# Optimization experiments

Measured on AMD Instinct MI355X. Metric: run time of the kernel, lower is better.

The kernel has to match this reference:

```python
import jax, jax.numpy as jnp
import numpy as np

V, D, H, L, FF, C = 32000, 512, 8, 3, 2048, 6
B, S = 32, 1024


def setup_inputs() -> dict:
    key = jax.random.key(0)
    ks = jax.random.split(key, 8)
    tokens = jax.random.randint(ks[0], (B, S), 0, V, dtype=jnp.int32)
    emb = jax.random.normal(ks[1], (V, D), dtype=jnp.float32) * 0.02
    qkv_w = jax.random.normal(ks[2], (L, D, 3 * D), dtype=jnp.float32) * (D ** -0.5)
    qkv_b = jnp.zeros((L, 3 * D), dtype=jnp.float32)
    fc_w = jax.random.normal(ks[3], (L, D, D), dtype=jnp.float32) * (D ** -0.5)
    fc_b = jnp.zeros((L, D), dtype=jnp.float32)
    gamma = jnp.ones((D,), dtype=jnp.float32)
    beta = jnp.zeros((D,), dtype=jnp.float32)
    fc1_w = jax.random.normal(ks[4], (D, FF), dtype=jnp.float32) * (D ** -0.5)
    fc1_b = jnp.zeros((FF,), dtype=jnp.float32)
    fc2_w = jax.random.normal(ks[5], (FF, C), dtype=jnp.float32) * (FF ** -0.5)
    fc2_b = jnp.zeros((C,), dtype=jnp.float32)
    return dict(tokens=tokens, emb=emb, qkv_w=qkv_w, qkv_b=qkv_b, fc_w=fc_w,
                fc_b=fc_b, gamma=gamma, beta=beta, fc1_w=fc1_w, fc1_b=fc1_b,
                fc2_w=fc2_w, fc2_b=fc2_b)


def _sinusoidal_pe(seq_len, dim):
    pos = jnp.arange(seq_len, dtype=jnp.float32)[:, None]
    div = jnp.exp(jnp.arange(0, dim, 2).astype(jnp.float32) * (-np.log(10000.0) / dim))
    pe = jnp.zeros((seq_len, dim), dtype=jnp.float32)
    pe = pe.at[:, 0::2].set(jnp.sin(pos * div))
    pe = pe.at[:, 1::2].set(jnp.cos(pos * div))
    return pe


def reference(tokens, emb, qkv_w, qkv_b, fc_w, fc_b, gamma, beta, fc1_w, fc1_b, fc2_w, fc2_b):
    b, s = tokens.shape
    dh = D // H
    scale = dh ** -0.5

    def layernorm(y):
        m = y.mean(-1, keepdims=True)
        v = ((y - m) ** 2).mean(-1, keepdims=True)
        return (y - m) * jax.lax.rsqrt(v + 1e-5) * gamma + beta

    x = emb[tokens] + _sinusoidal_pe(s, D)[None]  # [B,S,D]
    for l in range(L):
        qkv = (x @ qkv_w[l] + qkv_b[l]).reshape(b, s, H, 3, dh)
        q = qkv[..., 0, :].transpose(0, 2, 1, 3)  # [B,H,S,dh]
        k = qkv[..., 1, :].transpose(0, 2, 1, 3)
        v = qkv[..., 2, :].transpose(0, 2, 1, 3)
        attn = jax.nn.softmax(jnp.einsum('bhqd,bhkd->bhqk', q, k) * scale, axis=-1)
        o = jnp.einsum('bhqk,bhkd->bhqd', attn, v).transpose(0, 2, 1, 3).reshape(b, s, D)
        o = o @ fc_w[l] + fc_b[l]
        x = layernorm(o + x)
    pooled = x.mean(axis=1)  # [B,D]
    h = jax.nn.relu(pooled @ fc1_w + fc1_b)  # dropout is identity at inference
    return h @ fc2_w + fc2_b
```

## Files before the change

### kernel.cpp

```cpp
#include <hip/hip_runtime.h>
#include <cmath>

#define BS_TOK 32768
#define DMODEL 512
#define NHEAD 8
#define DHEAD 64
#define NLAYER 3
#define FFDIM 2048
#define NCLS 6
#define BATCH 32
#define SEQ 1024
#define QKVW 1536

typedef short short8 __attribute__((ext_vector_type(8)));
typedef float float4v __attribute__((ext_vector_type(4)));
typedef unsigned int uint4v __attribute__((ext_vector_type(4)));
#define MFMA_BF16 __builtin_amdgcn_mfma_f32_16x16x32_bf16
#define QSCALE 0.18033688011112042f

__device__ __forceinline__ unsigned short f2bf(float x) {
    return (unsigned short)((__float_as_uint(x) + 0x8000u) >> 16);
}

__device__ __forceinline__ unsigned int cvt_pk_bf16(float a, float b) {
    unsigned int r;
    asm("v_cvt_pk_bf16_f32 %0, %1, %2" : "=v"(r) : "v"(a), "v"(b));
    return r;
}

#define PL32(a, b) asm("v_permlane32_swap_b32 %0, %1" : "+v"(a), "+v"(b))
#define PL16(a, b) asm("v_permlane16_swap_b32 %0, %1" : "+v"(a), "+v"(b))

__global__ __launch_bounds__(128) void embed_pe_kernel(const int* __restrict__ tokens,
                                                       const float* __restrict__ emb,
                                                       float* __restrict__ X,
                                                       unsigned short* __restrict__ Xb) {
    int t = blockIdx.x;
    int pos = t & (SEQ - 1);
    int tok = tokens[t];
    int d0 = threadIdx.x * 4;
    float4 e = *(const float4*)(emb + (size_t)tok * DMODEL + d0);
    const float c = -9.210340371976184f / 512.0f;
    float div0 = expf((float)d0 * c);
    float div1 = expf((float)(d0 + 2) * c);
    float a0 = (float)pos * div0;
    float a1 = (float)pos * div1;
    e.x += sinf(a0); e.y += cosf(a0);
    e.z += sinf(a1); e.w += cosf(a1);
    *(float4*)(X + (size_t)t * DMODEL + d0) = e;
    *(ushort4*)(Xb + (size_t)t * DMODEL + d0) =
        make_ushort4(f2bf(e.x), f2bf(e.y), f2bf(e.z), f2bf(e.w));
}

__global__ __launch_bounds__(256) void transcvt_kernel(const float* __restrict__ in,
                                                       unsigned short* __restrict__ out,
                                                       int R, int C) {
    __shared__ float t[32][33];
    size_t base = (size_t)blockIdx.z * R * C;
    int c0 = blockIdx.x * 32, r0 = blockIdx.y * 32;
    int tx = threadIdx.x & 31, ty = threadIdx.x >> 5;
#pragma unroll
    for (int i = 0; i < 4; i++)
        t[ty + i * 8][tx] = in[base + (size_t)(r0 + ty + i * 8) * C + c0 + tx];
    __syncthreads();
#pragma unroll
    for (int i = 0; i < 4; i++)
        out[base + (size_t)(c0 + ty + i * 8) * R + r0 + tx] = f2bf(t[tx][ty + i * 8]);
}

__global__ __launch_bounds__(256) void transcvt_qkv_kernel(const float* __restrict__ in,
                                                           unsigned short* __restrict__ out) {
    __shared__ float t[32][33];
    int l = blockIdx.z;
    int n0 = blockIdx.x * 32, r0 = blockIdx.y * 32;
    int seg = n0 >> 9, nn = n0 & 511, h = nn >> 6, d0 = nn & 63;
    int c0 = h * 192 + seg * 64 + d0;
    float s = (seg == 0) ? QSCALE : 1.f;
    const float* inp = in + (size_t)l * DMODEL * QKVW;
    unsigned short* op = out + (size_t)l * QKVW * DMODEL;
    int tx = threadIdx.x & 31, ty = threadIdx.x >> 5;
#pragma unroll
    for (int i = 0; i < 4; i++)
        t[ty + i * 8][tx] = inp[(size_t)(r0 + ty + i * 8) * QKVW + c0 + tx];
    __syncthreads();
#pragma unroll
    for (int i = 0; i < 4; i++)
        op[(size_t)(n0 + ty + i * 8) * DMODEL + r0 + tx] = f2bf(t[tx][ty + i * 8] * s);
}

__global__ __launch_bounds__(256) void permbias_kernel(const float* __restrict__ qkv_b,
                                                       float* __restrict__ pb) {
    int i = blockIdx.x * 256 + threadIdx.x;
    int l = i / QKVW, n = i - l * QKVW;
    int seg = n >> 9, nn = n & 511, h = nn >> 6, d = nn & 63;
    float s = (seg == 0) ? QSCALE : 1.f;
    pb[i] = qkv_b[l * QKVW + h * 192 + seg * 64 + d] * s;
}

__global__ __launch_bounds__(256, 3) void gemm_qkv_kernel(const unsigned short* __restrict__ A,
                                                          const unsigned short* __restrict__ Bt,
                                                          const float* __restrict__ pb,
                                                          unsigned short* __restrict__ QKc,
                                                          unsigned short* __restrict__ Vt,
                                                          int M) {
    __shared__ unsigned short As[128 * 40];
    __shared__ unsigned short Bs[128 * 40];
    int bm = blockIdx.y * 128, bn = blockIdx.x * 128;
    int tid = threadIdx.x;
    int w = tid >> 6, lane = tid & 63, l15 = lane & 15, quad = lane >> 4;
    int wm = (w & 1) * 64, wn = (w >> 1) * 64;

    float4v acc[4][4];
    float4v z = {0.f, 0.f, 0.f, 0.f};
#pragma unroll
    for (int i = 0; i < 4; i++)
#pragma unroll
        for (int j = 0; j < 4; j++) acc[i][j] = z;

    int r0 = tid >> 2, o0 = (tid & 3) * 8;
    int r1 = (tid + 256) >> 2, o1 = (tid & 3) * 8;

    for (int k0 = 0; k0 < DMODEL; k0 += 32) {
        __syncthreads();
        *(short8*)&As[r0 * 40 + o0] = *(const short8*)(A + (size_t)(bm + r0) * DMODEL + k0 + o0);
        *(short8*)&As[r1 * 40 + o1] = *(const short8*)(A + (size_t)(bm + r1) * DMODEL + k0 + o1);
        *(short8*)&Bs[r0 * 40 + o0] = *(const short8*)(Bt + (size_t)(bn + r0) * DMODEL + k0 + o0);
        *(short8*)&Bs[r1 * 40 + o1] = *(const short8*)(Bt + (size_t)(bn + r1) * DMODEL + k0 + o1);
        __syncthreads();
        short8 af[4], bf[4];
#pragma unroll
        for (int i = 0; i < 4; i++)
            af[i] = *(short8*)&As[(wm + i * 16 + l15) * 40 + quad * 8];
#pragma unroll
        for (int j = 0; j < 4; j++)
            bf[j] = *(short8*)&Bs[(wn + j * 16 + l15) * 40 + quad * 8];
#pragma unroll
        for (int i = 0; i < 4; i++)
#pragma unroll
            for (int j = 0; j < 4; j++)
                acc[i][j] = MFMA_BF16(af[i], bf[j], acc[i][j], 0, 0, 0);
    }

    float bj[4];
#pragma unroll
    for (int j = 0; j < 4; j++) bj[j] = pb[bn + wn + j * 16 + l15];

    if (bn < 1024) {
#pragma unroll
        for (int i = 0; i < 4; i++)
#pragma unroll
            for (int r = 0; r < 4; r++) {
                size_t row = (size_t)(bm + wm + i * 16 + quad * 4 + r);
#pragma unroll
                for (int j = 0; j < 4; j++)
                    QKc[row * 1024 + bn + wn + j * 16 + l15] = f2bf(acc[i][j][r] + bj[j]);
            }
    } else {
        int bl = bm >> 10;
        int sbase = (bm & 1023) + wm;
#pragma unroll
        for (int j = 0; j < 4; j++) {
            int colp = bn - 1024 + wn + j * 16 + l15;
            int h = colp >> 6, d = colp & 63;
            unsigned short* vb = Vt + ((size_t)(bl * 8 + h) * 64 + d) * 1024 + sbase;
#pragma unroll
            for (int i = 0; i < 4; i++) {
                ushort4 v4 = make_ushort4(f2bf(acc[i][j][0] + bj[j]),
                                          f2bf(acc[i][j][1] + bj[j]),
                                          f2bf(acc[i][j][2] + bj[j]),
                                          f2bf(acc[i][j][3] + bj[j]));
                *(ushort4*)(vb + i * 16 + quad * 4) = v4;
            }
        }
    }
}

__global__ __launch_bounds__(256, 2) void attn_kernel(const unsigned short* __restrict__ QKc,
                                                      const unsigned short* __restrict__ Vt,
                                                      unsigned short* __restrict__ O) {
    __shared__ unsigned short Ks[64 * 72];
    __shared__ unsigned short Vts[64 * 72];
    int bh = blockIdx.y;
    int b = bh >> 3, h = bh & 7;
    int q0 = blockIdx.x * 256;
    int tid = threadIdx.x;
    int w = tid >> 6, lane = tid & 63, l15 = lane & 15, quad = lane >> 4;
    const unsigned short* Kg = QKc + (size_t)b * SEQ * 1024 + 512 + h * 64;
    const unsigned short* Vg = Vt + (size_t)bh * 64 * 1024;

    short8 qf[4][2];
#pragma unroll
    for (int i = 0; i < 4; i++) {
        const unsigned short* qb =
            QKc + (size_t)(b * SEQ + q0 + w * 64 + i * 16 + l15) * 1024 + h * 64;
        qf[i][0] = *(const short8*)(qb + quad * 8);
        qf[i][1] = *(const short8*)(qb + 32 + quad * 8);
    }

    float lsum[4] = {0.f, 0.f, 0.f, 0.f};
    float4v accO[4][4];
    float4v z = {0.f, 0.f, 0.f, 0.f};
#pragma unroll
    for (int i = 0; i < 4; i++)
#pragma unroll
        for (int dc = 0; dc < 4; dc++) accO[i][dc] = z;

    int sr = tid >> 2, so = (tid & 3) * 16;

    short8 kp0, kp1, vp0, vp1;
    {
        const unsigned short* kg = Kg + (size_t)sr * 1024 + so;
        kp0 = *(const short8*)kg;
        kp1 = *(const short8*)(kg + 8);
        const unsigned short* vg = Vg + (size_t)sr * 1024 + so;
        vp0 = *(const short8*)vg;
        vp1 = *(const short8*)(vg + 8);
    }

    for (int jt = 0; jt < SEQ / 64; jt++) {
        __syncthreads();
        *(short8*)&Ks[sr * 72 + so] = kp0;
        *(short8*)&Ks[sr * 72 + so + 8] = kp1;
        *(short8*)&Vts[sr * 72 + so] = vp0;
        *(short8*)&Vts[sr * 72 + so + 8] = vp1;
        __syncthreads();

        if (jt + 1 < SEQ / 64) {
            const unsigned short* kg = Kg + (size_t)((jt + 1) * 64 + sr) * 1024 + so;
            kp0 = *(const short8*)kg;
            kp1 = *(const short8*)(kg + 8);
            const unsigned short* vg = Vg + (size_t)sr * 1024 + (jt + 1) * 64 + so;
            vp0 = *(const short8*)vg;
            vp1 = *(const short8*)(vg + 8);
        }

        short8 pa[4][2];
#pragma unroll
        for (int f = 0; f < 2; f++) {
            float4v st[4][2];
#pragma unroll
            for (int jj = 0; jj < 2; jj++) {
                int jc = f * 2 + jj;
                short8 kf0 = *(short8*)&Ks[(jc * 16 + l15) * 72 + quad * 8];
                short8 kf1 = *(short8*)&Ks[(jc * 16 + l15) * 72 + 32 + quad * 8];
#pragma unroll
                for (int i = 0; i < 4; i++) {
                    float4v s0 = MFMA_BF16(kf0, qf[i][0], z, 0, 0, 0);
                    st[i][jj] = MFMA_BF16(kf1, qf[i][1], s0, 0, 0, 0);
                }
            }
#pragma unroll
            for (int i = 0; i < 4; i++) {
                unsigned int pk[4];
#pragma unroll
                for (int jj = 0; jj < 2; jj++) {
                    float p0 = exp2f(st[i][jj][0]);
                    float p1 = exp2f(st[i][jj][1]);
                    float p2 = exp2f(st[i][jj][2]);
                    float p3 = exp2f(st[i][jj][3]);
                    lsum[i] += (p0 + p1) + (p2 + p3);
                    pk[jj * 2 + 0] = cvt_pk_bf16(p0, p1);
                    pk[jj * 2 + 1] = cvt_pk_bf16(p2, p3);
                }
                PL32(pk[0], pk[2]);
                PL32(pk[1], pk[3]);
                PL16(pk[0], pk[2]);
                PL16(pk[1], pk[3]);
                uint4v t;
                t[0] = pk[0]; t[1] = pk[1]; t[2] = pk[2]; t[3] = pk[3];
                pa[i][f] = __builtin_bit_cast(short8, t);
            }
        }

        __builtin_amdgcn_s_setprio(1);
#pragma unroll
        for (int dc = 0; dc < 4; dc++) {
            short8 vf0 = *(short8*)&Vts[(dc * 16 + l15) * 72 + quad * 8];
            short8 vf1 = *(short8*)&Vts[(dc * 16 + l15) * 72 + 32 + quad * 8];
#pragma unroll
            for (int i = 0; i < 4; i++) {
                accO[i][dc] = MFMA_BF16(pa[i][0], vf0, accO[i][dc], 0, 0, 0);
                accO[i][dc] = MFMA_BF16(pa[i][1], vf1, accO[i][dc], 0, 0, 0);
            }
        }
        __builtin_amdgcn_s_setprio(0);
    }

#pragma unroll
    for (int i = 0; i < 4; i++) {
        float s = lsum[i];
        s += __shfl_xor(s, 16);
        s += __shfl_xor(s, 32);
#pragma unroll
        for (int r = 0; r < 4; r++) {
            float rinv = 1.f / __shfl(s, quad * 4 + r);
            size_t row = (size_t)(b * SEQ + q0 + w * 64 + i * 16 + quad * 4 + r);
#pragma unroll
            for (int dc = 0; dc < 4; dc++)
                O[row * DMODEL + h * DHEAD + dc * 16 + l15] = f2bf(accO[i][dc][r] * rinv);
        }
    }
}

__global__ __launch_bounds__(256, 2) void proj_ln_kernel(const unsigned short* __restrict__ A,
                                                         const unsigned short* __restrict__ Bt,
                                                         const float* __restrict__ bias,
                                                         const float* __restrict__ gamma,
                                                         const float* __restrict__ beta,
                                                         float* __restrict__ X,
                                                         unsigned short* __restrict__ Xb) {
    __shared__ unsigned short As[32 * 40];
    __shared__ unsigned short Bs[512 * 40];
    __shared__ float redS[4][32], redQ[4][32];
    int bm = blockIdx.x * 32;
    int tid = threadIdx.x;
    int w = tid >> 6, lane = tid & 63, l15 = lane & 15, quad = lane >> 4;
    int wn = w * 128;

    float4v acc[2][8];
    float4v z = {0.f, 0.f, 0.f, 0.f};
#pragma unroll
    for (int i = 0; i < 2; i++)
#pragma unroll
        for (int j = 0; j < 8; j++) acc[i][j] = z;

    for (int k0 = 0; k0 < DMODEL; k0 += 32) {
        __syncthreads();
        if (tid < 128) {
            int r = tid >> 2, o = (tid & 3) * 8;
            *(short8*)&As[r * 40 + o] = *(const short8*)(A + (size_t)(bm + r) * DMODEL + k0 + o);
        }
#pragma unroll
        for (int u = 0; u < 8; u++) {
            int c = tid + u * 256;
            int r = c >> 2, o = (c & 3) * 8;
            *(short8*)&Bs[r * 40 + o] = *(const short8*)(Bt + (size_t)r * DMODEL + k0 + o);
        }
        __syncthreads();
        short8 af[2];
#pragma unroll
        for (int i = 0; i < 2; i++)
            af[i] = *(short8*)&As[(i * 16 + l15) * 40 + quad * 8];
#pragma unroll
        for (int j = 0; j < 8; j++) {
            short8 bf = *(short8*)&Bs[(wn + j * 16 + l15) * 40 + quad * 8];
            acc[0][j] = MFMA_BF16(af[0], bf, acc[0][j], 0, 0, 0);
            acc[1][j] = MFMA_BF16(af[1], bf, acc[1][j], 0, 0, 0);
        }
    }

    float bj[8], g[8], be[8];
#pragma unroll
    for (int j = 0; j < 8; j++) {
        int col = wn + j * 16 + l15;
        bj[j] = bias[col]; g[j] = gamma[col]; be[j] = beta[col];
    }

    float o[2][4][8];
#pragma unroll
    for (int i = 0; i < 2; i++)
#pragma unroll
        for (int r = 0; r < 4; r++) {
            int lrow = i * 16 + quad * 4 + r;
            size_t row = (size_t)(bm + lrow);
            float ss = 0.f, qq = 0.f;
#pragma unroll
            for (int j = 0; j < 8; j++) {
                float v = acc[i][j][r] + bj[j] + X[row * DMODEL + wn + j * 16 + l15];
                o[i][r][j] = v; ss += v; qq += v * v;
            }
#pragma unroll
            for (int mask = 1; mask < 16; mask <<= 1) {
                ss += __shfl_xor(ss, mask);
                qq += __shfl_xor(qq, mask);
            }
            if (l15 == 0) { redS[w][lrow] = ss; redQ[w][lrow] = qq; }
        }
    __syncthreads();
#pragma unroll
    for (int i = 0; i < 2; i++)
#pragma unroll
        for (int r = 0; r < 4; r++) {
            int lrow = i * 16 + quad * 4 + r;
            float S = redS[0][lrow] + redS[1][lrow] + redS[2][lrow] + redS[3][lrow];
            float Q = redQ[0][lrow] + redQ[1][lrow] + redQ[2][lrow] + redQ[3][lrow];
            float mean = S * (1.f / 512.f);
            float var = Q * (1.f / 512.f) - mean * mean;
            float rstd = rsqrtf(var + 1e-5f);
            size_t row = (size_t)(bm + lrow);
#pragma unroll
            for (int j = 0; j < 8; j++) {
                float n = (o[i][r][j] - mean) * rstd * g[j] + be[j];
                X[row * DMODEL + wn + j * 16 + l15] = n;
                Xb[row * DMODEL + wn + j * 16 + l15] = f2bf(n);
            }
        }
}

__global__ __launch_bounds__(256) void zero_kernel(float* __restrict__ p) {
    p[blockIdx.x * 256 + threadIdx.x] = 0.f;
}
__global__ __launch_bounds__(128) void pool_kernel(const float* __restrict__ X,
                                                   float* __restrict__ pooled) {
    int b = blockIdx.x, ch = blockIdx.y;
    int d0 = threadIdx.x * 4;
    float4 acc = make_float4(0.f, 0.f, 0.f, 0.f);
    const float* base = X + (size_t)(b * SEQ + ch * 64) * DMODEL + d0;
    for (int s2 = 0; s2 < 64; s2++) {
        float4 v = *(const float4*)(base + (size_t)s2 * DMODEL);
        acc.x += v.x; acc.y += v.y; acc.z += v.z; acc.w += v.w;
    }
    atomicAdd(pooled + b * DMODEL + d0 + 0, acc.x);
    atomicAdd(pooled + b * DMODEL + d0 + 1, acc.y);
    atomicAdd(pooled + b * DMODEL + d0 + 2, acc.z);
    atomicAdd(pooled + b * DMODEL + d0 + 3, acc.w);
}

__global__ __launch_bounds__(256) void fc1_kernel(const float* __restrict__ pooled,
                                                  const float* __restrict__ fc1_w,
                                                  const float* __restrict__ fc1_b,
                                                  float* __restrict__ h) {
    __shared__ float p[DMODEL];
    int ffc = blockIdx.x, b = blockIdx.y;
    int tid = threadIdx.x;
    p[tid] = pooled[b * DMODEL + tid] * (1.f / 1024.f);
    p[tid + 256] = pooled[b * DMODEL + tid + 256] * (1.f / 1024.f);
    __syncthreads();
    int ff = ffc * 256 + tid;
    float acc = fc1_b[ff];
    for (int k = 0; k < DMODEL; k++) acc += p[k] * fc1_w[(size_t)k * FFDIM + ff];
    h[(size_t)b * FFDIM + ff] = fmaxf(acc, 0.f);
}

__global__ __launch_bounds__(256) void fc2_kernel(const float* __restrict__ h,
                                                  const float* __restrict__ fc2_w,
                                                  const float* __restrict__ fc2_b,
                                                  float* __restrict__ out) {
    __shared__ float red[NCLS][256];
    int b = blockIdx.x, tid = threadIdx.x;
    float a[NCLS];
#pragma unroll
    for (int c = 0; c < NCLS; c++) a[c] = 0.f;
    int k0 = tid * 8;
#pragma unroll
    for (int u = 0; u < 8; u++) {
        float hv = h[(size_t)b * FFDIM + k0 + u];
#pragma unroll
        for (int c = 0; c < NCLS; c++) a[c] += hv * fc2_w[(k0 + u) * NCLS + c];
    }
#pragma unroll
    for (int c = 0; c < NCLS; c++) red[c][tid] = a[c];
    __syncthreads();
    if (tid < NCLS) {
        float s = 0.f;
        for (int i = 0; i < 256; i++) s += red[tid][i];
        out[b * NCLS + tid] = s + fc2_b[tid];
    }
}

extern "C" void kernel_launch(void* const* d_in, const int* in_sizes, int n_in,
                              void* d_out, int out_size, void* d_ws, size_t ws_size,
                              hipStream_t stream) {
    const int* tokens = (const int*)d_in[0];
    const float* emb = (const float*)d_in[1];
    const float* qkv_w = (const float*)d_in[2];
    const float* qkv_b = (const float*)d_in[3];
    const float* fc_w = (const float*)d_in[4];
    const float* fc_b = (const float*)d_in[5];
    const float* gamma = (const float*)d_in[6];
    const float* beta = (const float*)d_in[7];
    const float* fc1_w = (const float*)d_in[8];
    const float* fc1_b = (const float*)d_in[9];
    const float* fc2_w = (const float*)d_in[10];
    const float* fc2_b = (const float*)d_in[11];
    float* out = (float*)d_out;

    char* p = (char*)d_ws;
    float* X = (float*)p;                         p += (size_t)BS_TOK * DMODEL * 4;
    unsigned short* Xb = (unsigned short*)p;      p += (size_t)BS_TOK * DMODEL * 2;
    float* pooled = (float*)p;                    p += (size_t)BATCH * DMODEL * 4;
    float* hbuf = (float*)p;                      p += (size_t)BATCH * FFDIM * 4;
    float* pb = (float*)p;                        p += (size_t)NLAYER * QKVW * 4;
    unsigned short* qkv_wbt = (unsigned short*)p; p += (size_t)NLAYER * QKVW * DMODEL * 2;
    unsigned short* fc_wt = (unsigned short*)p;   p += (size_t)NLAYER * DMODEL * DMODEL * 2;
    size_t fixed_bytes = (size_t)(p - (char*)d_ws);
    size_t per_batch = (size_t)SEQ * 1024 * 2 + (size_t)NHEAD * 64 * SEQ * 2
                     + (size_t)SEQ * DMODEL * 2;
    int chunkB = 1;
    for (int cb = 32; cb >= 1; cb >>= 1)
        if (fixed_bytes + (size_t)cb * per_batch <= ws_size) { chunkB = cb; break; }
    unsigned short* QKc = (unsigned short*)p;     p += (size_t)chunkB * SEQ * 1024 * 2;
    unsigned short* Vt = (unsigned short*)p;      p += (size_t)chunkB * NHEAD * 64 * SEQ * 2;
    unsigned short* Oc = (unsigned short*)p;
    int rows = chunkB * SEQ;
    int nchunks = BATCH / chunkB;

    embed_pe_kernel<<<BS_TOK, 128, 0, stream>>>(tokens, emb, X, Xb);
    permbias_kernel<<<NLAYER * QKVW / 256, 256, 0, stream>>>(qkv_b, pb);
    transcvt_qkv_kernel<<<dim3(QKVW / 32, DMODEL / 32, NLAYER), 256, 0, stream>>>(
        qkv_w, qkv_wbt);
    transcvt_kernel<<<dim3(DMODEL / 32, DMODEL / 32, NLAYER), 256, 0, stream>>>(
        fc_w, fc_wt, DMODEL, DMODEL);

    for (int l = 0; l < NLAYER; l++) {
        for (int c = 0; c < nchunks; c++) {
            unsigned short* Xbc = Xb + (size_t)c * rows * DMODEL;
            float* Xc = X + (size_t)c * rows * DMODEL;
            gemm_qkv_kernel<<<dim3(QKVW / 128, rows / 128), 256, 0, stream>>>(
                Xbc, qkv_wbt + (size_t)l * QKVW * DMODEL, pb + (size_t)l * QKVW,
                QKc, Vt, rows);
            attn_kernel<<<dim3(SEQ / 256, chunkB * NHEAD), 256, 0, stream>>>(QKc, Vt, Oc);
            proj_ln_kernel<<<rows / 32, 256, 0, stream>>>(
                Oc, fc_wt + (size_t)l * DMODEL * DMODEL, fc_b + (size_t)l * DMODEL,
                gamma, beta, Xc, Xbc);
        }
    }

    zero_kernel<<<BATCH * DMODEL / 256, 256, 0, stream>>>(pooled);
    pool_kernel<<<dim3(BATCH, 16), 128, 0, stream>>>(X, pooled);
    fc1_kernel<<<dim3(FFDIM / 256, BATCH), 256, 0, stream>>>(pooled, fc1_w, fc1_b, hbuf);
    fc2_kernel<<<BATCH, 256, 0, stream>>>(hbuf, fc2_w, fc2_b, out);
}
```

Baseline: 941.4 us.

## Double-buffer LDS in QKV GEMM and attention, interleave softmax with PV MFMAs

```diff
diff --git a/kernel.cpp b/kernel.cpp
--- a/kernel.cpp
+++ b/kernel.cpp
@@ -103,8 +103,8 @@
                                                           unsigned short* __restrict__ QKc,
                                                           unsigned short* __restrict__ Vt,
                                                           int M) {
-    __shared__ unsigned short As[128 * 40];
-    __shared__ unsigned short Bs[128 * 40];
+    __shared__ unsigned short As[2][128 * 40];
+    __shared__ unsigned short Bs[2][128 * 40];
     int bm = blockIdx.y * 128, bn = blockIdx.x * 128;
     int tid = threadIdx.x;
     int w = tid >> 6, lane = tid & 63, l15 = lane & 15, quad = lane >> 4;
@@ -118,27 +118,45 @@
         for (int j = 0; j < 4; j++) acc[i][j] = z;
 
     int r0 = tid >> 2, o0 = (tid & 3) * 8;
-    int r1 = (tid + 256) >> 2, o1 = (tid & 3) * 8;
+    int r1 = (tid + 256) >> 2;
+
+    const unsigned short* Ar0 = A + (size_t)(bm + r0) * DMODEL + o0;
+    const unsigned short* Ar1 = A + (size_t)(bm + r1) * DMODEL + o0;
+    const unsigned short* Br0 = Bt + (size_t)(bn + r0) * DMODEL + o0;
+    const unsigned short* Br1 = Bt + (size_t)(bn + r1) * DMODEL + o0;
+
+    short8 a0 = *(const short8*)Ar0;
+    short8 a1 = *(const short8*)Ar1;
+    short8 b0 = *(const short8*)Br0;
+    short8 b1 = *(const short8*)Br1;
 
     for (int k0 = 0; k0 < DMODEL; k0 += 32) {
+        unsigned short* Ac = As[(k0 >> 5) & 1];
+        unsigned short* Bc = Bs[(k0 >> 5) & 1];
+        *(short8*)&Ac[r0 * 40 + o0] = a0;
+        *(short8*)&Ac[r1 * 40 + o0] = a1;
+        *(short8*)&Bc[r0 * 40 + o0] = b0;
+        *(short8*)&Bc[r1 * 40 + o0] = b1;
         __syncthreads();
-        *(short8*)&As[r0 * 40 + o0] = *(const short8*)(A + (size_t)(bm + r0) * DMODEL + k0 + o0);
-        *(short8*)&As[r1 * 40 + o1] = *(const short8*)(A + (size_t)(bm + r1) * DMODEL + k0 + o1);
-        *(short8*)&Bs[r0 * 40 + o0] = *(const short8*)(Bt + (size_t)(bn + r0) * DMODEL + k0 + o0);
-        *(short8*)&Bs[r1 * 40 + o1] = *(const short8*)(Bt + (size_t)(bn + r1) * DMODEL + k0 + o1);
-        __syncthreads();
+        int kn = (k0 + 32 < DMODEL) ? k0 + 32 : k0;
+        a0 = *(const short8*)(Ar0 + kn);
+        a1 = *(const short8*)(Ar1 + kn);
+        b0 = *(const short8*)(Br0 + kn);
+        b1 = *(const short8*)(Br1 + kn);
         short8 af[4], bf[4];
 #pragma unroll
         for (int i = 0; i < 4; i++)
-            af[i] = *(short8*)&As[(wm + i * 16 + l15) * 40 + quad * 8];
+            af[i] = *(short8*)&Ac[(wm + i * 16 + l15) * 40 + quad * 8];
 #pragma unroll
         for (int j = 0; j < 4; j++)
-            bf[j] = *(short8*)&Bs[(wn + j * 16 + l15) * 40 + quad * 8];
+            bf[j] = *(short8*)&Bc[(wn + j * 16 + l15) * 40 + quad * 8];
+        __builtin_amdgcn_s_setprio(1);
 #pragma unroll
         for (int i = 0; i < 4; i++)
 #pragma unroll
             for (int j = 0; j < 4; j++)
                 acc[i][j] = MFMA_BF16(af[i], bf[j], acc[i][j], 0, 0, 0);
+        __builtin_amdgcn_s_setprio(0);
     }
 
     float bj[4];
@@ -178,8 +196,8 @@
 __global__ __launch_bounds__(256, 2) void attn_kernel(const unsigned short* __restrict__ QKc,
                                                       const unsigned short* __restrict__ Vt,
                                                       unsigned short* __restrict__ O) {
-    __shared__ unsigned short Ks[64 * 72];
-    __shared__ unsigned short Vts[64 * 72];
+    __shared__ unsigned short Ks[2][64 * 72];
+    __shared__ unsigned short Vts[2][64 * 72];
     int bh = blockIdx.y;
     int b = bh >> 3, h = bh & 7;
     int q0 = blockIdx.x * 256;
@@ -217,71 +235,115 @@
         vp1 = *(const short8*)(vg + 8);
     }
 
-    for (int jt = 0; jt < SEQ / 64; jt++) {
+    const int NT = SEQ / 64;
+    for (int jt = 0; jt < NT; jt++) {
+        unsigned short* Kc = Ks[jt & 1];
+        unsigned short* Vc = Vts[jt & 1];
+        *(short8*)&Kc[sr * 72 + so] = kp0;
+        *(short8*)&Kc[sr * 72 + so + 8] = kp1;
+        *(short8*)&Vc[sr * 72 + so] = vp0;
+        *(short8*)&Vc[sr * 72 + so + 8] = vp1;
         __syncthreads();
-        *(short8*)&Ks[sr * 72 + so] = kp0;
-        *(short8*)&Ks[sr * 72 + so + 8] = kp1;
-        *(short8*)&Vts[sr * 72 + so] = vp0;
-        *(short8*)&Vts[sr * 72 + so + 8] = vp1;
-        __syncthreads();
-
-        if (jt + 1 < SEQ / 64) {
-            const unsigned short* kg = Kg + (size_t)((jt + 1) * 64 + sr) * 1024 + so;
+
+        {
+            int nj = (jt + 1 < NT) ? jt + 1 : jt;
+            const unsigned short* kg = Kg + (size_t)(nj * 64 + sr) * 1024 + so;
             kp0 = *(const short8*)kg;
             kp1 = *(const short8*)(kg + 8);
-            const unsigned short* vg = Vg + (size_t)sr * 1024 + (jt + 1) * 64 + so;
+            const unsigned short* vg = Vg + (size_t)sr * 1024 + nj * 64 + so;
             vp0 = *(const short8*)vg;
             vp1 = *(const short8*)(vg + 8);
         }
 
-        short8 pa[4][2];
-#pragma unroll
-        for (int f = 0; f < 2; f++) {
-            float4v st[4][2];
+        float4v st0[4][2];
+        __builtin_amdgcn_s_setprio(1);
+#pragma unroll
+        for (int jj = 0; jj < 2; jj++) {
+            short8 kf0 = *(short8*)&Kc[(jj * 16 + l15) * 72 + quad * 8];
+            short8 kf1 = *(short8*)&Kc[(jj * 16 + l15) * 72 + 32 + quad * 8];
+#pragma unroll
+            for (int i = 0; i < 4; i++) {
+                float4v s0 = MFMA_BF16(kf0, qf[i][0], z, 0, 0, 0);
+                st0[i][jj] = MFMA_BF16(kf1, qf[i][1], s0, 0, 0, 0);
+            }
+        }
+        __builtin_amdgcn_s_setprio(0);
+
+        short8 pa0[4];
+#pragma unroll
+        for (int i = 0; i < 4; i++) {
+            unsigned int pk[4];
 #pragma unroll
             for (int jj = 0; jj < 2; jj++) {
-                int jc = f * 2 + jj;
-                short8 kf0 = *(short8*)&Ks[(jc * 16 + l15) * 72 + quad * 8];
-                short8 kf1 = *(short8*)&Ks[(jc * 16 + l15) * 72 + 32 + quad * 8];
-#pragma unroll
-                for (int i = 0; i < 4; i++) {
-                    float4v s0 = MFMA_BF16(kf0, qf[i][0], z, 0, 0, 0);
-                    st[i][jj] = MFMA_BF16(kf1, qf[i][1], s0, 0, 0, 0);
-                }
-            }
+                float p0 = exp2f(st0[i][jj][0]);
+                float p1 = exp2f(st0[i][jj][1]);
+                float p2 = exp2f(st0[i][jj][2]);
+                float p3 = exp2f(st0[i][jj][3]);
+                lsum[i] += (p0 + p1) + (p2 + p3);
+                pk[jj * 2 + 0] = cvt_pk_bf16(p0, p1);
+                pk[jj * 2 + 1] = cvt_pk_bf16(p2, p3);
+            }
+            PL32(pk[0], pk[2]);
+            PL32(pk[1], pk[3]);
+            PL16(pk[0], pk[2]);
+            PL16(pk[1], pk[3]);
+            uint4v t;
+            t[0] = pk[0]; t[1] = pk[1]; t[2] = pk[2]; t[3] = pk[3];
+            pa0[i] = __builtin_bit_cast(short8, t);
+        }
+
+        float4v st1[4][2];
+        __builtin_amdgcn_s_setprio(1);
+#pragma unroll
+        for (int jj = 0; jj < 2; jj++) {
+            short8 kf0 = *(short8*)&Kc[((2 + jj) * 16 + l15) * 72 + quad * 8];
+            short8 kf1 = *(short8*)&Kc[((2 + jj) * 16 + l15) * 72 + 32 + quad * 8];
 #pragma unroll
             for (int i = 0; i < 4; i++) {
-                unsigned int pk[4];
-#pragma unroll
-                for (int jj = 0; jj < 2; jj++) {
-                    float p0 = exp2f(st[i][jj][0]);
-                    float p1 = exp2f(st[i][jj][1]);
-                    float p2 = exp2f(st[i][jj][2]);
-                    float p3 = exp2f(st[i][jj][3]);
-                    lsum[i] += (p0 + p1) + (p2 + p3);
-                    pk[jj * 2 + 0] = cvt_pk_bf16(p0, p1);
-                    pk[jj * 2 + 1] = cvt_pk_bf16(p2, p3);
-                }
-                PL32(pk[0], pk[2]);
-                PL32(pk[1], pk[3]);
-                PL16(pk[0], pk[2]);
-                PL16(pk[1], pk[3]);
-                uint4v t;
-                t[0] = pk[0]; t[1] = pk[1]; t[2] = pk[2]; t[3] = pk[3];
-                pa[i][f] = __builtin_bit_cast(short8, t);
-            }
+                float4v s0 = MFMA_BF16(kf0, qf[i][0], z, 0, 0, 0);
+                st1[i][jj] = MFMA_BF16(kf1, qf[i][1], s0, 0, 0, 0);
+            }
+        }
+
+#pragma unroll
+        for (int dc = 0; dc < 4; dc++) {
+            short8 vf0 = *(short8*)&Vc[(dc * 16 + l15) * 72 + quad * 8];
+#pragma unroll
+            for (int i = 0; i < 4; i++)
+                accO[i][dc] = MFMA_BF16(pa0[i], vf0, accO[i][dc], 0, 0, 0);
+        }
+        __builtin_amdgcn_s_setprio(0);
+
+        short8 pa1[4];
+#pragma unroll
+        for (int i = 0; i < 4; i++) {
+            unsigned int pk[4];
+#pragma unroll
+            for (int jj = 0; jj < 2; jj++) {
+                float p0 = exp2f(st1[i][jj][0]);
+                float p1 = exp2f(st1[i][jj][1]);
+                float p2 = exp2f(st1[i][jj][2]);
+                float p3 = exp2f(st1[i][jj][3]);
+                lsum[i] += (p0 + p1) + (p2 + p3);
+                pk[jj * 2 + 0] = cvt_pk_bf16(p0, p1);
+                pk[jj * 2 + 1] = cvt_pk_bf16(p2, p3);
+            }
+            PL32(pk[0], pk[2]);
+            PL32(pk[1], pk[3]);
+            PL16(pk[0], pk[2]);
+            PL16(pk[1], pk[3]);
+            uint4v t;
+            t[0] = pk[0]; t[1] = pk[1]; t[2] = pk[2]; t[3] = pk[3];
+            pa1[i] = __builtin_bit_cast(short8, t);
         }
 
         __builtin_amdgcn_s_setprio(1);
 #pragma unroll
         for (int dc = 0; dc < 4; dc++) {
-            short8 vf0 = *(short8*)&Vts[(dc * 16 + l15) * 72 + quad * 8];
-            short8 vf1 = *(short8*)&Vts[(dc * 16 + l15) * 72 + 32 + quad * 8];
-#pragma unroll
-            for (int i = 0; i < 4; i++) {
-                accO[i][dc] = MFMA_BF16(pa[i][0], vf0, accO[i][dc], 0, 0, 0);
-                accO[i][dc] = MFMA_BF16(pa[i][1], vf1, accO[i][dc], 0, 0, 0);
-            }
+            short8 vf1 = *(short8*)&Vc[(dc * 16 + l15) * 72 + 32 + quad * 8];
+#pragma unroll
+            for (int i = 0; i < 4; i++)
+                accO[i][dc] = MFMA_BF16(pa1[i], vf1, accO[i][dc], 0, 0, 0);
         }
         __builtin_amdgcn_s_setprio(0);
     }
```

After: 929.7 us. No clear change (-1.2%).

## Double-buffer QKV and proj GEMM tiles via direct global-to-LDS loads

Applied to the files above, without the earlier changes.

```diff
diff --git a/kernel.cpp b/kernel.cpp
--- a/kernel.cpp
+++ b/kernel.cpp
@@ -30,6 +30,12 @@
 
 #define PL32(a, b) asm("v_permlane32_swap_b32 %0, %1" : "+v"(a), "+v"(b))
 #define PL16(a, b) asm("v_permlane16_swap_b32 %0, %1" : "+v"(a), "+v"(b))
+
+__device__ __forceinline__ void gload16(const unsigned short* g, unsigned short* l) {
+    __builtin_amdgcn_global_load_lds(
+        (const __attribute__((address_space(1))) unsigned int*)g,
+        (__attribute__((address_space(3))) unsigned int*)l, 16, 0, 0);
+}
 
 __global__ __launch_bounds__(128) void embed_pe_kernel(const int* __restrict__ tokens,
                                                        const float* __restrict__ emb,
@@ -103,8 +109,8 @@
                                                           unsigned short* __restrict__ QKc,
                                                           unsigned short* __restrict__ Vt,
                                                           int M) {
-    __shared__ unsigned short As[128 * 40];
-    __shared__ unsigned short Bs[128 * 40];
+    __shared__ unsigned short As[2][128 * 32];
+    __shared__ unsigned short Bs[2][128 * 32];
     int bm = blockIdx.y * 128, bn = blockIdx.x * 128;
     int tid = threadIdx.x;
     int w = tid >> 6, lane = tid & 63, l15 = lane & 15, quad = lane >> 4;
@@ -117,28 +123,46 @@
 #pragma unroll
         for (int j = 0; j < 4; j++) acc[i][j] = z;
 
-    int r0 = tid >> 2, o0 = (tid & 3) * 8;
-    int r1 = (tid + 256) >> 2, o1 = (tid & 3) * 8;
-
-    for (int k0 = 0; k0 < DMODEL; k0 += 32) {
-        __syncthreads();
-        *(short8*)&As[r0 * 40 + o0] = *(const short8*)(A + (size_t)(bm + r0) * DMODEL + k0 + o0);
-        *(short8*)&As[r1 * 40 + o1] = *(const short8*)(A + (size_t)(bm + r1) * DMODEL + k0 + o1);
-        *(short8*)&Bs[r0 * 40 + o0] = *(const short8*)(Bt + (size_t)(bn + r0) * DMODEL + k0 + o0);
-        *(short8*)&Bs[r1 * 40 + o1] = *(const short8*)(Bt + (size_t)(bn + r1) * DMODEL + k0 + o1);
-        __syncthreads();
+    int sr0 = w * 16 + (lane >> 2);
+    int sr1 = (w + 4) * 16 + (lane >> 2);
+    int sc = ((lane & 3) ^ ((lane >> 3) & 3)) * 8;
+    const unsigned short* Ag = A + (size_t)bm * DMODEL;
+    const unsigned short* Bg = Bt + (size_t)bn * DMODEL;
+
+    gload16(Ag + (size_t)sr0 * DMODEL + sc, &As[0][w * 512]);
+    gload16(Ag + (size_t)sr1 * DMODEL + sc, &As[0][(w + 4) * 512]);
+    gload16(Bg + (size_t)sr0 * DMODEL + sc, &Bs[0][w * 512]);
+    gload16(Bg + (size_t)sr1 * DMODEL + sc, &Bs[0][(w + 4) * 512]);
+    __syncthreads();
+
+    int sw = (l15 >> 1) & 3;
+    for (int kt = 0; kt < 16; kt++) {
+        const unsigned short* Ac = As[kt & 1];
+        const unsigned short* Bc = Bs[kt & 1];
+        if (kt + 1 < 16) {
+            int kn = (kt + 1) * 32;
+            unsigned short* An = (unsigned short*)As[(kt + 1) & 1];
+            unsigned short* Bn = (unsigned short*)Bs[(kt + 1) & 1];
+            gload16(Ag + (size_t)sr0 * DMODEL + kn + sc, &An[w * 512]);
+            gload16(Ag + (size_t)sr1 * DMODEL + kn + sc, &An[(w + 4) * 512]);
+            gload16(Bg + (size_t)sr0 * DMODEL + kn + sc, &Bn[w * 512]);
+            gload16(Bg + (size_t)sr1 * DMODEL + kn + sc, &Bn[(w + 4) * 512]);
+        }
         short8 af[4], bf[4];
 #pragma unroll
         for (int i = 0; i < 4; i++)
-            af[i] = *(short8*)&As[(wm + i * 16 + l15) * 40 + quad * 8];
+            af[i] = *(short8*)&Ac[(wm + i * 16 + l15) * 32 + (quad ^ sw) * 8];
 #pragma unroll
         for (int j = 0; j < 4; j++)
-            bf[j] = *(short8*)&Bs[(wn + j * 16 + l15) * 40 + quad * 8];
+            bf[j] = *(short8*)&Bc[(wn + j * 16 + l15) * 32 + (quad ^ sw) * 8];
+        __builtin_amdgcn_s_setprio(1);
 #pragma unroll
         for (int i = 0; i < 4; i++)
 #pragma unroll
             for (int j = 0; j < 4; j++)
                 acc[i][j] = MFMA_BF16(af[i], bf[j], acc[i][j], 0, 0, 0);
+        __builtin_amdgcn_s_setprio(0);
+        __syncthreads();
     }
 
     float bj[4];
@@ -309,8 +333,8 @@
                                                          const float* __restrict__ beta,
                                                          float* __restrict__ X,
                                                          unsigned short* __restrict__ Xb) {
-    __shared__ unsigned short As[32 * 40];
-    __shared__ unsigned short Bs[512 * 40];
+    __shared__ unsigned short As2[2][32 * 32];
+    __shared__ unsigned short Bs2[2][512 * 32];
     __shared__ float redS[4][32], redQ[4][32];
     int bm = blockIdx.x * 32;
     int tid = threadIdx.x;
@@ -324,29 +348,48 @@
 #pragma unroll
         for (int j = 0; j < 8; j++) acc[i][j] = z;
 
-    for (int k0 = 0; k0 < DMODEL; k0 += 32) {
-        __syncthreads();
-        if (tid < 128) {
-            int r = tid >> 2, o = (tid & 3) * 8;
-            *(short8*)&As[r * 40 + o] = *(const short8*)(A + (size_t)(bm + r) * DMODEL + k0 + o);
-        }
-#pragma unroll
-        for (int u = 0; u < 8; u++) {
-            int c = tid + u * 256;
-            int r = c >> 2, o = (c & 3) * 8;
-            *(short8*)&Bs[r * 40 + o] = *(const short8*)(Bt + (size_t)r * DMODEL + k0 + o);
-        }
-        __syncthreads();
+    int lrow4 = lane >> 2;
+    int sc = ((lane & 3) ^ ((lane >> 3) & 3)) * 8;
+    const unsigned short* Ag = A + (size_t)bm * DMODEL;
+
+    if (w < 2)
+        gload16(Ag + (size_t)(w * 16 + lrow4) * DMODEL + sc, &As2[0][w * 512]);
+#pragma unroll
+    for (int u = 0; u < 8; u++) {
+        int ch = w * 8 + u;
+        gload16(Bt + (size_t)(ch * 16 + lrow4) * DMODEL + sc, &Bs2[0][ch * 512]);
+    }
+    __syncthreads();
+
+    int sw = (l15 >> 1) & 3;
+    for (int kt = 0; kt < 16; kt++) {
+        const unsigned short* Ac = As2[kt & 1];
+        const unsigned short* Bc = Bs2[kt & 1];
+        if (kt + 1 < 16) {
+            int kn = (kt + 1) * 32;
+            unsigned short* An = (unsigned short*)As2[(kt + 1) & 1];
+            unsigned short* Bn = (unsigned short*)Bs2[(kt + 1) & 1];
+            if (w < 2)
+                gload16(Ag + (size_t)(w * 16 + lrow4) * DMODEL + kn + sc, &An[w * 512]);
+#pragma unroll
+            for (int u = 0; u < 8; u++) {
+                int ch = w * 8 + u;
+                gload16(Bt + (size_t)(ch * 16 + lrow4) * DMODEL + kn + sc, &Bn[ch * 512]);
+            }
+        }
         short8 af[2];
 #pragma unroll
         for (int i = 0; i < 2; i++)
-            af[i] = *(short8*)&As[(i * 16 + l15) * 40 + quad * 8];
+            af[i] = *(short8*)&Ac[(i * 16 + l15) * 32 + (quad ^ sw) * 8];
+        __builtin_amdgcn_s_setprio(1);
 #pragma unroll
         for (int j = 0; j < 8; j++) {
-            short8 bf = *(short8*)&Bs[(wn + j * 16 + l15) * 40 + quad * 8];
+            short8 bf = *(short8*)&Bc[(wn + j * 16 + l15) * 32 + (quad ^ sw) * 8];
             acc[0][j] = MFMA_BF16(af[0], bf, acc[0][j], 0, 0, 0);
             acc[1][j] = MFMA_BF16(af[1], bf, acc[1][j], 0, 0, 0);
         }
+        __builtin_amdgcn_s_setprio(0);
+        __syncthreads();
     }
 
     float bj[8], g[8], be[8];
```

After: 904.4 us. 1.04x faster.
